# Kernel tuning notes

Measured on AMD Instinct MI355X. Metric: run time of the kernel, lower is better.

The kernel has to match this reference:

```python
import jax, jax.numpy as jnp
import numpy as np
from math import sqrt

ALPHA = 1.0
EPS = 1e-8


def setup_inputs() -> dict:
    key = jax.random.key(0)
    k1, k2, k3 = jax.random.split(key, 3)
    B, L, S, H, E = 4, 2048, 2048, 16, 64
    queries = jax.random.normal(k1, (B, L, H, E), dtype=jnp.float32)
    keys = jax.random.normal(k2, (B, S, H, E), dtype=jnp.float32)
    values = jax.random.normal(k3, (B, S, H, E), dtype=jnp.float32)
    return {"queries": queries, "keys": keys, "values": values}


def reference(queries, keys, values):
    B, L, H, E = queries.shape
    scale = 1.0 / sqrt(E)
    # dot product scores: [B,H,L,S]
    dot = jnp.einsum('blhe,bshe->bhls', queries, keys)
    # squared norms: [B,H,L,1] and [B,H,1,S]
    qn2 = jnp.sum(queries * queries, axis=-1).transpose(0, 2, 1)[..., :, None]
    kn2 = jnp.sum(keys * keys, axis=-1).transpose(0, 2, 1)[..., None, :]
    # wedge (parallelogram area) norm^2 = |q|^2|k|^2 - (q.k)^2, clipped at 0
    wedge_norm = jnp.sqrt(jax.nn.relu(qn2 * kn2 - dot * dot) + EPS)
    scores = ((1.0 - ALPHA) * dot + ALPHA * wedge_norm) * scale
    A = jax.nn.softmax(scores, axis=-1)  # no mask (mask_flag=False), dropout=0
    V = jnp.einsum('bhls,bshd->blhd', A, values)
    return V, jnp.mean(jnp.abs(scores))
```

## Files before the change

kernel.cpp:

```cpp
#include <hip/hip_runtime.h>
#include <math.h>

constexpr int Bb = 4, Ll = 2048, Ss = 2048, Hh = 16, Ee = 64;
constexpr float SCALE = 0.125f;
constexpr float EPSV  = 1e-8f;
constexpr float S2E   = 0.125f * 1.44269504089f;
constexpr float INV_CNT = 1.0f / (4.0f * 16.0f * 2048.0f * 2048.0f);

typedef __attribute__((ext_vector_type(8))) short  short8;
typedef __attribute__((ext_vector_type(4))) float  floatx4;

#define MFMA __builtin_amdgcn_mfma_f32_16x16x32_bf16

#define GLL(gp, lp)                                                        \
  __builtin_amdgcn_global_load_lds(                                        \
      (const __attribute__((address_space(1))) unsigned int*)(gp),         \
      (__attribute__((address_space(3))) unsigned int*)(lp), 16, 0, 0)

__device__ __forceinline__ short f2bf(float f) {
  unsigned u = __builtin_bit_cast(unsigned, f);
  u += 0x7fffu + ((u >> 16) & 1u);
  return (short)(u >> 16);
}
__device__ __forceinline__ float sq4(float4 v) {
  return v.x * v.x + v.y * v.y + v.z * v.z + v.w * v.w;
}
__device__ __forceinline__ short8 pack8(float4 x, float4 y) {
  short8 r;
  r[0] = f2bf(x.x); r[1] = f2bf(x.y); r[2] = f2bf(x.z); r[3] = f2bf(x.w);
  r[4] = f2bf(y.x); r[5] = f2bf(y.y); r[6] = f2bf(y.z); r[7] = f2bf(y.w);
  return r;
}

__global__ __launch_bounds__(256) void geom_pre_kernel(
    const float* __restrict__ Kg, const float* __restrict__ Vg,
    short* __restrict__ Kbf, short* __restrict__ Vtg,
    float* __restrict__ kn2g, float* __restrict__ sumg) {
  __shared__ short Vl[64][72];
  const int tid = threadIdx.x;
  const int bid = blockIdx.x;
  const int st = bid & 31, h = (bid >> 5) & 15, b = bid >> 9;
  const int s0 = st * 64;
  const int r64 = tid >> 2, ec = (tid & 3) * 16;
  const int bh = b * 16 + h;

  if (bid == 0 && tid == 0) *sumg = 0.0f;

  const float4* kp = (const float4*)(Kg + (((size_t)b * Ss + s0 + r64) * Hh + h) * Ee + ec);
  float4 k0 = kp[0], k1 = kp[1], k2 = kp[2], k3 = kp[3];
  float kn = sq4(k0) + sq4(k1) + sq4(k2) + sq4(k3);
  kn += __shfl_xor(kn, 1);
  kn += __shfl_xor(kn, 2);
  if ((tid & 3) == 0) kn2g[(size_t)bh * Ss + s0 + r64] = kn;
  short* ko = Kbf + ((size_t)bh * Ss + s0 + r64) * Ee + ec;
  *(short8*)(ko)     = pack8(k0, k1);
  *(short8*)(ko + 8) = pack8(k2, k3);

  const float4* vp = (const float4*)(Vg + (((size_t)b * Ss + s0 + r64) * Hh + h) * Ee + ec);
  float4 v0 = vp[0], v1 = vp[1], v2 = vp[2], v3 = vp[3];
  *(short8*)(&Vl[r64][ec])     = pack8(v0, v1);
  *(short8*)(&Vl[r64][ec + 8]) = pack8(v2, v3);
  __syncthreads();
  const int e = tid >> 2, sc = (tid & 3) * 16;
  short8 t0, t1;
#pragma unroll
  for (int j = 0; j < 8; ++j) {
    t0[j] = Vl[sc + j][e];
    t1[j] = Vl[sc + 8 + j][e];
  }
  short* vo = Vtg + ((size_t)bh * Ee + e) * Ss + s0 + sc;
  *(short8*)(vo)     = t0;
  *(short8*)(vo + 8) = t1;
}

constexpr int VOFF = 8192, POFF = 16384, LWOFF = 25600, RDOFF = 25856;

__global__ __launch_bounds__(256, 6) void geom_attn_kernel(
    const float* __restrict__ Qg, const short* __restrict__ Kbf,
    const short* __restrict__ Vtg, const float* __restrict__ kn2g,
    float* __restrict__ outg, float* __restrict__ sumg) {
  __shared__ __align__(16) char smem[25872];

  const int tid  = threadIdx.x;
  const int w    = tid >> 6;
  const int lane = tid & 63;
  const int c    = lane & 15;
  const int q4   = lane >> 4;

  const int bid = blockIdx.x;
  const int lt = bid & 31, h = (bid >> 5) & 15, b = bid >> 9;
  const int l0 = lt * 64 + w * 16;
  const int bh = b * 16 + h;

  const float4* qp = (const float4*)(Qg + (((size_t)b * Ll + (l0 + c)) * Hh + h) * Ee);
  float4 a0 = qp[2 * q4], a1 = qp[2 * q4 + 1];
  float4 a2 = qp[8 + 2 * q4], a3 = qp[9 + 2 * q4];
  float qn = sq4(a0) + sq4(a1) + sq4(a2) + sq4(a3);
  qn += __shfl_xor(qn, 16);
  qn += __shfl_xor(qn, 32);
  const float qn2v = qn;
  short8 qb0 = pack8(a0, a1);
  short8 qb1 = pack8(a2, a3);

  const int Gl = w * 128 + lane;
  const int rK = Gl >> 3, pK = Gl & 7;
  const int gK = pK ^ (rK & 7);
  const char* kSrc = (const char*)Kbf + (size_t)bh * Ss * 128 + rK * 128 + gK * 16;
  const char* vSrc = (const char*)Vtg + (size_t)bh * Ee * 4096 + rK * 4096 + gK * 16;
  char* kDst = smem + w * 2048;
  char* vDst = smem + VOFF + w * 2048;

  const float4* knp = (const float4*)(kn2g + (size_t)bh * Ss) + q4;

  const int addrA0 = c * 128 + ((q4 ^ (c & 7)) << 4);
  const int addrA1 = addrA0 ^ 64;
  const char* pKa0 = smem + addrA0;
  const char* pKa1 = smem + addrA1;
  char* pPw  = smem + POFF + w * 2304;
  char* pPwr = pPw + c * 144 + q4 * 8;
  const char* pPrd = pPw + c * 144 + q4 * 16;
  float* lw = (float*)(smem + LWOFF + w * 64);
  float* red = (float*)(smem + RDOFF);

  floatx4 o0 = {0.f, 0.f, 0.f, 0.f}, o1 = o0, o2 = o0, o3 = o0;
  float lp = 0.0f, scsum = 0.0f;

  for (int s0 = 0; s0 < Ss; s0 += 64) {
    __syncthreads();
    GLL(kSrc, kDst);
    GLL(kSrc + 1024, kDst + 1024);
    GLL(vSrc, vDst);
    GLL(vSrc + 32768, vDst + 1024);
    kSrc += 8192;
    vSrc += 128;
    __syncthreads();

#pragma unroll
    for (int ct = 0; ct < 4; ++ct) {
      short8 ka0 = *(const short8*)(pKa0 + ct * 2048);
      short8 ka1 = *(const short8*)(pKa1 + ct * 2048);
      floatx4 d = {0.f, 0.f, 0.f, 0.f};
      d = MFMA(ka0, qb0, d, 0, 0, 0);
      d = MFMA(ka1, qb1, d, 0, 0, 0);
      float4 knv = knp[(s0 >> 2) + ct * 4];
      float p[4];
#pragma unroll
      for (int r = 0; r < 4; ++r) {
        float dot = d[r];
        float w2 = fmaf(-dot, dot, qn2v * (&knv.x)[r]);
        w2 = fmaxf(w2, EPSV);
        float rt = __builtin_amdgcn_sqrtf(w2);
        scsum += rt;
        float pe = __builtin_amdgcn_exp2f(rt * S2E);
        lp += pe;
        p[r] = pe;
      }
      uint2 pk;
      pk.x = __builtin_amdgcn_perm(__builtin_bit_cast(unsigned, p[1]),
                                   __builtin_bit_cast(unsigned, p[0]), 0x07060302u);
      pk.y = __builtin_amdgcn_perm(__builtin_bit_cast(unsigned, p[3]),
                                   __builtin_bit_cast(unsigned, p[2]), 0x07060302u);
      *(uint2*)(pPwr + ct * 32) = pk;
    }

#pragma unroll
    for (int kc = 0; kc < 2; ++kc) {
      short8 pa = *(const short8*)(pPrd + kc * 64);
      const char* vb = (kc == 0 ? pKa0 : pKa1) + VOFF;
      short8 v0 = *(const short8*)(vb);
      short8 v1 = *(const short8*)(vb + 2048);
      short8 v2 = *(const short8*)(vb + 4096);
      short8 v3 = *(const short8*)(vb + 6144);
      o0 = MFMA(pa, v0, o0, 0, 0, 0);
      o1 = MFMA(pa, v1, o1, 0, 0, 0);
      o2 = MFMA(pa, v2, o2, 0, 0, 0);
      o3 = MFMA(pa, v3, o3, 0, 0, 0);
    }
  }

  lp += __shfl_xor(lp, 16);
  lp += __shfl_xor(lp, 32);
  if (lane < 16) lw[lane] = lp;
  __syncthreads();
  float4 lv = *(const float4*)((const char*)lw + q4 * 16);

#pragma unroll
  for (int r = 0; r < 4; ++r) {
    float inv = 1.0f / (&lv.x)[r];
    int row = l0 + q4 * 4 + r;
    float* orow = outg + (((size_t)b * Ll + row) * Hh + h) * Ee;
    orow[0 + c]  = o0[r] * inv;
    orow[16 + c] = o1[r] * inv;
    orow[32 + c] = o2[r] * inv;
    orow[48 + c] = o3[r] * inv;
  }

  scsum += __shfl_xor(scsum, 1);
  scsum += __shfl_xor(scsum, 2);
  scsum += __shfl_xor(scsum, 4);
  scsum += __shfl_xor(scsum, 8);
  scsum += __shfl_xor(scsum, 16);
  scsum += __shfl_xor(scsum, 32);
  if (lane == 0) red[w] = scsum;
  __syncthreads();
  if (tid == 0) {
    float s = red[0] + red[1] + red[2] + red[3];
    atomicAdd(sumg, s * (SCALE * INV_CNT));
  }
}

extern "C" void kernel_launch(void* const* d_in, const int* in_sizes, int n_in,
                              void* d_out, int out_size, void* d_ws, size_t ws_size,
                              hipStream_t stream) {
  const float* Q = (const float*)d_in[0];
  const float* K = (const float*)d_in[1];
  const float* V = (const float*)d_in[2];
  float* out   = (float*)d_out;
  float* sumsc = out + (size_t)Bb * Ll * Hh * Ee;

  short* Kbf = (short*)d_ws;
  short* Vtg = Kbf + (size_t)Bb * Hh * Ss * Ee;
  float* kn2 = (float*)(Vtg + (size_t)Bb * Hh * Ee * Ss);

  hipLaunchKernelGGL(geom_pre_kernel, dim3(Bb * Hh * (Ss / 64)), dim3(256), 0,
                     stream, K, V, Kbf, Vtg, kn2, sumsc);
  hipLaunchKernelGGL(geom_attn_kernel, dim3(Bb * Hh * (Ll / 64)), dim3(256), 0,
                     stream, Q, Kbf, Vtg, kn2, out, sumsc);
}
```

Measured before the change: 273.8 us.

## Double-buffer K/V tiles, process 32 query rows per wave, prescale Q

The attention kernel now handles 128 query rows per block, 32 per wave in two MFMA groups, so each K/V tile loaded into LDS is reused across twice as many queries. K/V tiles of 32 keys are double-buffered with async global-to-LDS loads, which removes one barrier per iteration and overlaps loads with compute. Q is prescaled by scale*log2e so the exp2 needs no extra multiply, and the key norms are staged in LDS. The V transpose in the prep kernel now goes directly through registers instead of shared memory, and the block-level score reduction becomes per-wave atomics. Register pressure rises, and occupancy drops to a launch bound of 4 blocks.

```diff
diff --git a/kernel.cpp b/kernel.cpp
--- a/kernel.cpp
+++ b/kernel.cpp
@@ -2,50 +2,51 @@
 #include <math.h>
 
 constexpr int Bb = 4, Ll = 2048, Ss = 2048, Hh = 16, Ee = 64;
-constexpr float SCALE = 0.125f;
-constexpr float EPSV  = 1e-8f;
-constexpr float S2E   = 0.125f * 1.44269504089f;
+constexpr float S2E  = 0.125f * 1.44269504088896341f;
+constexpr float EPS2 = 1e-8f * S2E * S2E;
 constexpr float INV_CNT = 1.0f / (4.0f * 16.0f * 2048.0f * 2048.0f);
+constexpr float SUM_SCALE = INV_CNT * 0.69314718055994531f;
 
 typedef __attribute__((ext_vector_type(8))) short  short8;
 typedef __attribute__((ext_vector_type(4))) float  floatx4;
 
 #define MFMA __builtin_amdgcn_mfma_f32_16x16x32_bf16
 
-#define GLL(gp, lp)                                                        \
+#define GLL(gp, lp_)                                                       \
   __builtin_amdgcn_global_load_lds(                                        \
       (const __attribute__((address_space(1))) unsigned int*)(gp),         \
-      (__attribute__((address_space(3))) unsigned int*)(lp), 16, 0, 0)
-
-__device__ __forceinline__ short f2bf(float f) {
+      (__attribute__((address_space(3))) unsigned int*)(lp_), 16, 0, 0)
+
+__device__ __forceinline__ unsigned bfrnd(float f) {
   unsigned u = __builtin_bit_cast(unsigned, f);
-  u += 0x7fffu + ((u >> 16) & 1u);
-  return (short)(u >> 16);
+  return u + 0x7fffu + ((u >> 16) & 1u);
 }
 __device__ __forceinline__ float sq4(float4 v) {
   return v.x * v.x + v.y * v.y + v.z * v.z + v.w * v.w;
 }
+__device__ __forceinline__ float4 mul4(float4 v, float s) {
+  float4 r; r.x = v.x * s; r.y = v.y * s; r.z = v.z * s; r.w = v.w * s;
+  return r;
+}
 __device__ __forceinline__ short8 pack8(float4 x, float4 y) {
-  short8 r;
-  r[0] = f2bf(x.x); r[1] = f2bf(x.y); r[2] = f2bf(x.z); r[3] = f2bf(x.w);
-  r[4] = f2bf(y.x); r[5] = f2bf(y.y); r[6] = f2bf(y.z); r[7] = f2bf(y.w);
-  return r;
+  union { short8 s; unsigned u[4]; } r;
+  r.u[0] = __builtin_amdgcn_perm(bfrnd(x.y), bfrnd(x.x), 0x07060302u);
+  r.u[1] = __builtin_amdgcn_perm(bfrnd(x.w), bfrnd(x.z), 0x07060302u);
+  r.u[2] = __builtin_amdgcn_perm(bfrnd(y.y), bfrnd(y.x), 0x07060302u);
+  r.u[3] = __builtin_amdgcn_perm(bfrnd(y.w), bfrnd(y.z), 0x07060302u);
+  return r.s;
 }
 
 __global__ __launch_bounds__(256) void geom_pre_kernel(
     const float* __restrict__ Kg, const float* __restrict__ Vg,
     short* __restrict__ Kbf, short* __restrict__ Vtg,
     float* __restrict__ kn2g, float* __restrict__ sumg) {
-  __shared__ short Vl[64][72];
-  const int tid = threadIdx.x;
-  const int bid = blockIdx.x;
+  const int tid = threadIdx.x, bid = blockIdx.x;
   const int st = bid & 31, h = (bid >> 5) & 15, b = bid >> 9;
-  const int s0 = st * 64;
+  const int s0 = st * 64, bh = b * 16 + h;
+  if (bid == 0 && tid == 0) *sumg = 0.0f;
+
   const int r64 = tid >> 2, ec = (tid & 3) * 16;
-  const int bh = b * 16 + h;
-
-  if (bid == 0 && tid == 0) *sumg = 0.0f;
-
   const float4* kp = (const float4*)(Kg + (((size_t)b * Ss + s0 + r64) * Hh + h) * Ee + ec);
   float4 k0 = kp[0], k1 = kp[1], k2 = kp[2], k3 = kp[3];
   float kn = sq4(k0) + sq4(k1) + sq4(k2) + sq4(k3);
@@ -56,143 +57,153 @@
   *(short8*)(ko)     = pack8(k0, k1);
   *(short8*)(ko + 8) = pack8(k2, k3);
 
-  const float4* vp = (const float4*)(Vg + (((size_t)b * Ss + s0 + r64) * Hh + h) * Ee + ec);
-  float4 v0 = vp[0], v1 = vp[1], v2 = vp[2], v3 = vp[3];
-  *(short8*)(&Vl[r64][ec])     = pack8(v0, v1);
-  *(short8*)(&Vl[r64][ec + 8]) = pack8(v2, v3);
-  __syncthreads();
-  const int e = tid >> 2, sc = (tid & 3) * 16;
-  short8 t0, t1;
-#pragma unroll
-  for (int j = 0; j < 8; ++j) {
-    t0[j] = Vl[sc + j][e];
-    t1[j] = Vl[sc + 8 + j][e];
-  }
-  short* vo = Vtg + ((size_t)bh * Ee + e) * Ss + s0 + sc;
-  *(short8*)(vo)     = t0;
-  *(short8*)(vo + 8) = t1;
-}
-
-constexpr int VOFF = 8192, POFF = 16384, LWOFF = 25600, RDOFF = 25856;
-
-__global__ __launch_bounds__(256, 6) void geom_attn_kernel(
+  const int sq = tid >> 4, eq = tid & 15;
+  const float* vb = Vg + (((size_t)b * Ss + s0 + sq * 4) * Hh + h) * Ee + eq * 4;
+  float4 r0 = *(const float4*)(vb);
+  float4 r1 = *(const float4*)(vb + Hh * Ee);
+  float4 r2 = *(const float4*)(vb + 2 * Hh * Ee);
+  float4 r3 = *(const float4*)(vb + 3 * Hh * Ee);
+  short* vo = Vtg + ((size_t)bh * Ee + eq * 4) * Ss + s0 + sq * 4;
+#pragma unroll
+  for (int j = 0; j < 4; ++j) {
+    uint2 t;
+    t.x = __builtin_amdgcn_perm(bfrnd((&r1.x)[j]), bfrnd((&r0.x)[j]), 0x07060302u);
+    t.y = __builtin_amdgcn_perm(bfrnd((&r3.x)[j]), bfrnd((&r2.x)[j]), 0x07060302u);
+    *(uint2*)(vo + (size_t)j * Ss) = t;
+  }
+}
+
+constexpr int KB0 = 0, VB0 = 8192, PB = 16384, KN2 = 24576;
+
+__global__ __launch_bounds__(256, 4) void geom_attn_kernel(
     const float* __restrict__ Qg, const short* __restrict__ Kbf,
     const short* __restrict__ Vtg, const float* __restrict__ kn2g,
     float* __restrict__ outg, float* __restrict__ sumg) {
-  __shared__ __align__(16) char smem[25872];
-
-  const int tid  = threadIdx.x;
-  const int w    = tid >> 6;
-  const int lane = tid & 63;
-  const int c    = lane & 15;
-  const int q4   = lane >> 4;
-
+  __shared__ __align__(16) char smem[32768];
+
+  const int tid = threadIdx.x, w = tid >> 6, lane = tid & 63;
+  const int c = lane & 15, q4 = lane >> 4;
   const int bid = blockIdx.x;
-  const int lt = bid & 31, h = (bid >> 5) & 15, b = bid >> 9;
-  const int l0 = lt * 64 + w * 16;
+  const int lt = bid & 15, h = (bid >> 4) & 15, b = bid >> 8;
   const int bh = b * 16 + h;
-
-  const float4* qp = (const float4*)(Qg + (((size_t)b * Ll + (l0 + c)) * Hh + h) * Ee);
-  float4 a0 = qp[2 * q4], a1 = qp[2 * q4 + 1];
-  float4 a2 = qp[8 + 2 * q4], a3 = qp[9 + 2 * q4];
-  float qn = sq4(a0) + sq4(a1) + sq4(a2) + sq4(a3);
-  qn += __shfl_xor(qn, 16);
-  qn += __shfl_xor(qn, 32);
-  const float qn2v = qn;
-  short8 qb0 = pack8(a0, a1);
-  short8 qb1 = pack8(a2, a3);
-
-  const int Gl = w * 128 + lane;
-  const int rK = Gl >> 3, pK = Gl & 7;
-  const int gK = pK ^ (rK & 7);
-  const char* kSrc = (const char*)Kbf + (size_t)bh * Ss * 128 + rK * 128 + gK * 16;
-  const char* vSrc = (const char*)Vtg + (size_t)bh * Ee * 4096 + rK * 4096 + gK * 16;
-  char* kDst = smem + w * 2048;
-  char* vDst = smem + VOFF + w * 2048;
-
-  const float4* knp = (const float4*)(kn2g + (size_t)bh * Ss) + q4;
-
-  const int addrA0 = c * 128 + ((q4 ^ (c & 7)) << 4);
-  const int addrA1 = addrA0 ^ 64;
-  const char* pKa0 = smem + addrA0;
-  const char* pKa1 = smem + addrA1;
-  char* pPw  = smem + POFF + w * 2304;
-  char* pPwr = pPw + c * 144 + q4 * 8;
-  const char* pPrd = pPw + c * 144 + q4 * 16;
-  float* lw = (float*)(smem + LWOFF + w * 64);
-  float* red = (float*)(smem + RDOFF);
-
-  floatx4 o0 = {0.f, 0.f, 0.f, 0.f}, o1 = o0, o2 = o0, o3 = o0;
-  float lp = 0.0f, scsum = 0.0f;
-
-  for (int s0 = 0; s0 < Ss; s0 += 64) {
+  const int l0 = lt * 128 + w * 32;
+
+  short8 qb[2][2];
+  float qn2v[2];
+#pragma unroll
+  for (int g = 0; g < 2; ++g) {
+    const float4* qp = (const float4*)(Qg + (((size_t)b * Ll + l0 + g * 16 + c) * Hh + h) * Ee);
+    float4 a0 = mul4(qp[2 * q4], S2E),     a1 = mul4(qp[2 * q4 + 1], S2E);
+    float4 a2 = mul4(qp[8 + 2 * q4], S2E), a3 = mul4(qp[9 + 2 * q4], S2E);
+    float qn = sq4(a0) + sq4(a1) + sq4(a2) + sq4(a3);
+    qn += __shfl_xor(qn, 16);
+    qn += __shfl_xor(qn, 32);
+    qn2v[g] = qn;
+    qb[g][0] = pack8(a0, a1);
+    qb[g][1] = pack8(a2, a3);
+  }
+
+  const int rK = tid >> 3, pK = tid & 7;
+  const char* kSrc = (const char*)Kbf + (size_t)bh * (Ss * 128) + rK * 128 + ((pK ^ (rK & 7)) * 16);
+  const int eV = tid >> 2;
+  const char* vSrc = (const char*)Vtg + (size_t)bh * (Ss * 128) + eV * (Ss * 2) + (((tid & 3) ^ (eV & 3)) * 16);
+  char* kDstW = smem + KB0 + w * 1024;
+  char* vDstW = smem + VB0 + w * 1024;
+
+  {
+    const char* knSrc = (const char*)kn2g + (size_t)bh * 8192 + (size_t)tid * 16;
+    GLL(knSrc, smem + KN2 + w * 1024);
+    GLL(knSrc + 4096, smem + KN2 + w * 1024 + 4096);
+  }
+
+  GLL(kSrc, kDstW);
+  GLL(vSrc, vDstW);
+  kSrc += 4096;
+  vSrc += 64;
+
+  floatx4 o[2][4] = {};
+  float lp0 = 0.f, lp1 = 0.f, scsum = 0.f;
+
+  const int kOff = c * 128 + ((q4 ^ (c & 7)) * 16);
+  const int vOff = c * 64 + ((q4 ^ (c & 3)) * 16);
+  const int pRd  = PB + w * 2048 + c * 64 + ((q4 ^ (c & 3)) * 16);
+  const int pWrB = PB + w * 2048 + c * 64 + (q4 & 1) * 8;
+  const int knRd = KN2 + q4 * 16;
+
+  for (int it = 0; it < 64; ++it) {
+    const int p = it & 1;
     __syncthreads();
-    GLL(kSrc, kDst);
-    GLL(kSrc + 1024, kDst + 1024);
-    GLL(vSrc, vDst);
-    GLL(vSrc + 32768, vDst + 1024);
-    kSrc += 8192;
-    vSrc += 128;
-    __syncthreads();
-
-#pragma unroll
-    for (int ct = 0; ct < 4; ++ct) {
-      short8 ka0 = *(const short8*)(pKa0 + ct * 2048);
-      short8 ka1 = *(const short8*)(pKa1 + ct * 2048);
-      floatx4 d = {0.f, 0.f, 0.f, 0.f};
-      d = MFMA(ka0, qb0, d, 0, 0, 0);
-      d = MFMA(ka1, qb1, d, 0, 0, 0);
-      float4 knv = knp[(s0 >> 2) + ct * 4];
-      float p[4];
-#pragma unroll
-      for (int r = 0; r < 4; ++r) {
-        float dot = d[r];
-        float w2 = fmaf(-dot, dot, qn2v * (&knv.x)[r]);
-        w2 = fmaxf(w2, EPSV);
-        float rt = __builtin_amdgcn_sqrtf(w2);
-        scsum += rt;
-        float pe = __builtin_amdgcn_exp2f(rt * S2E);
-        lp += pe;
-        p[r] = pe;
+    GLL(kSrc, kDstW + (p ^ 1) * 4096);
+    GLL(vSrc, vDstW + (p ^ 1) * 4096);
+    kSrc += 4096;
+    vSrc += 64;
+
+    const char* Kb = smem + KB0 + p * 4096;
+    const char* Vb = smem + VB0 + p * 4096;
+
+#pragma unroll
+    for (int ct = 0; ct < 2; ++ct) {
+      short8 ka0 = *(const short8*)(Kb + ct * 2048 + kOff);
+      short8 ka1 = *(const short8*)(Kb + ct * 2048 + (kOff ^ 64));
+      float4 knv = *(const float4*)(smem + knRd + it * 128 + ct * 64);
+      const int pwCT = ((ct * 2 + (q4 >> 1)) ^ (c & 3)) * 16;
+#pragma unroll
+      for (int g = 0; g < 2; ++g) {
+        floatx4 d = {0.f, 0.f, 0.f, 0.f};
+        d = MFMA(ka0, qb[g][0], d, 0, 0, 0);
+        d = MFMA(ka1, qb[g][1], d, 0, 0, 0);
+        float pe[4];
+#pragma unroll
+        for (int r = 0; r < 4; ++r) {
+          float dot = d[r];
+          float w2 = fmaf(-dot, dot, qn2v[g] * (&knv.x)[r]);
+          w2 = fmaxf(w2, EPS2);
+          float rt = __builtin_amdgcn_sqrtf(w2);
+          scsum += rt;
+          float e = __builtin_amdgcn_exp2f(rt);
+          if (g == 0) lp0 += e; else lp1 += e;
+          pe[r] = e;
+        }
+        uint2 pk;
+        pk.x = __builtin_amdgcn_perm(__builtin_bit_cast(unsigned, pe[1]),
+                                     __builtin_bit_cast(unsigned, pe[0]), 0x07060302u);
+        pk.y = __builtin_amdgcn_perm(__builtin_bit_cast(unsigned, pe[3]),
+                                     __builtin_bit_cast(unsigned, pe[2]), 0x07060302u);
+        *(uint2*)(smem + pWrB + g * 1024 + pwCT) = pk;
       }
-      uint2 pk;
-      pk.x = __builtin_amdgcn_perm(__builtin_bit_cast(unsigned, p[1]),
-                                   __builtin_bit_cast(unsigned, p[0]), 0x07060302u);
-      pk.y = __builtin_amdgcn_perm(__builtin_bit_cast(unsigned, p[3]),
-                                   __builtin_bit_cast(unsigned, p[2]), 0x07060302u);
-      *(uint2*)(pPwr + ct * 32) = pk;
     }
 
-#pragma unroll
-    for (int kc = 0; kc < 2; ++kc) {
-      short8 pa = *(const short8*)(pPrd + kc * 64);
-      const char* vb = (kc == 0 ? pKa0 : pKa1) + VOFF;
-      short8 v0 = *(const short8*)(vb);
-      short8 v1 = *(const short8*)(vb + 2048);
-      short8 v2 = *(const short8*)(vb + 4096);
-      short8 v3 = *(const short8*)(vb + 6144);
-      o0 = MFMA(pa, v0, o0, 0, 0, 0);
-      o1 = MFMA(pa, v1, o1, 0, 0, 0);
-      o2 = MFMA(pa, v2, o2, 0, 0, 0);
-      o3 = MFMA(pa, v3, o3, 0, 0, 0);
+    short8 vb0 = *(const short8*)(Vb + vOff);
+    short8 vb1 = *(const short8*)(Vb + 1024 + vOff);
+    short8 vb2 = *(const short8*)(Vb + 2048 + vOff);
+    short8 vb3 = *(const short8*)(Vb + 3072 + vOff);
+#pragma unroll
+    for (int g = 0; g < 2; ++g) {
+      short8 pa = *(const short8*)(smem + pRd + g * 1024);
+      o[g][0] = MFMA(pa, vb0, o[g][0], 0, 0, 0);
+      o[g][1] = MFMA(pa, vb1, o[g][1], 0, 0, 0);
+      o[g][2] = MFMA(pa, vb2, o[g][2], 0, 0, 0);
+      o[g][3] = MFMA(pa, vb3, o[g][3], 0, 0, 0);
     }
   }
 
-  lp += __shfl_xor(lp, 16);
-  lp += __shfl_xor(lp, 32);
-  if (lane < 16) lw[lane] = lp;
   __syncthreads();
-  float4 lv = *(const float4*)((const char*)lw + q4 * 16);
-
-#pragma unroll
-  for (int r = 0; r < 4; ++r) {
-    float inv = 1.0f / (&lv.x)[r];
-    int row = l0 + q4 * 4 + r;
-    float* orow = outg + (((size_t)b * Ll + row) * Hh + h) * Ee;
-    orow[0 + c]  = o0[r] * inv;
-    orow[16 + c] = o1[r] * inv;
-    orow[32 + c] = o2[r] * inv;
-    orow[48 + c] = o3[r] * inv;
+
+  lp0 += __shfl_xor(lp0, 16); lp0 += __shfl_xor(lp0, 32);
+  lp1 += __shfl_xor(lp1, 16); lp1 += __shfl_xor(lp1, 32);
+
+#pragma unroll
+  for (int g = 0; g < 2; ++g) {
+    float lpg = (g == 0) ? lp0 : lp1;
+#pragma unroll
+    for (int r = 0; r < 4; ++r) {
+      float inv = 1.0f / __shfl(lpg, q4 * 4 + r);
+      float* orow = outg + (((size_t)b * Ll + l0 + g * 16 + q4 * 4 + r) * Hh + h) * Ee;
+      orow[c]      = o[g][0][r] * inv;
+      orow[16 + c] = o[g][1][r] * inv;
+      orow[32 + c] = o[g][2][r] * inv;
+      orow[48 + c] = o[g][3][r] * inv;
+    }
   }
 
   scsum += __shfl_xor(scsum, 1);
@@ -201,12 +212,7 @@
   scsum += __shfl_xor(scsum, 8);
   scsum += __shfl_xor(scsum, 16);
   scsum += __shfl_xor(scsum, 32);
-  if (lane == 0) red[w] = scsum;
-  __syncthreads();
-  if (tid == 0) {
-    float s = red[0] + red[1] + red[2] + red[3];
-    atomicAdd(sumg, s * (SCALE * INV_CNT));
-  }
+  if (lane == 0) atomicAdd(sumg, scsum * SUM_SCALE);
 }
 
 extern "C" void kernel_launch(void* const* d_in, const int* in_sizes, int n_in,
@@ -224,6 +230,6 @@
 
   hipLaunchKernelGGL(geom_pre_kernel, dim3(Bb * Hh * (Ss / 64)), dim3(256), 0,
                      stream, K, V, Kbf, Vtg, kn2, sumsc);
-  hipLaunchKernelGGL(geom_attn_kernel, dim3(Bb * Hh * (Ll / 64)), dim3(256), 0,
+  hipLaunchKernelGGL(geom_attn_kernel, dim3(Bb * Hh * (Ll / 128)), dim3(256), 0,
                      stream, Q, Kbf, Vtg, kn2, out, sumsc);
 }
```

New measurement: 266.4 us. -2.7%, faster.
